# Kernel tuning notes

Hardware: AMD Instinct MI355X
Metric: run time of the kernel (lower is better)

## Reference

```python
import jax, jax.numpy as jnp
import numpy as np

N_NODES = 50000
N_EDGES = 800000
D = 128
N_GRAPHS = 64
N_CLASSES = 10


def setup_inputs() -> dict:
    key = jax.random.key(0)
    ks = jax.random.split(key, 10)
    x = jax.random.normal(ks[0], (N_NODES, D), dtype=jnp.float32)
    edge_index = jax.random.randint(ks[1], (2, N_EDGES), 0, N_NODES, dtype=jnp.int64)
    batch = jnp.sort(jax.random.randint(ks[2], (N_NODES,), 0, N_GRAPHS, dtype=jnp.int64))
    s = 1.0 / np.sqrt(D)
    W1a = jax.random.uniform(ks[3], (D, D), jnp.float32, -s, s)
    W1b = jax.random.uniform(ks[4], (D, D), jnp.float32, -s, s)
    W2a = jax.random.uniform(ks[5], (D, D), jnp.float32, -s, s)
    W2b = jax.random.uniform(ks[6], (D, D), jnp.float32, -s, s)
    Wfc = jax.random.uniform(ks[7], (D, N_CLASSES), jnp.float32, -s, s)
    return {
        "x": x, "edge_index": edge_index, "batch": batch,
        "W1a": W1a, "b1a": jnp.zeros((D,), jnp.float32),
        "W1b": W1b, "b1b": jnp.zeros((D,), jnp.float32),
        "W2a": W2a, "b2a": jnp.zeros((D,), jnp.float32),
        "W2b": W2b, "b2b": jnp.zeros((D,), jnp.float32),
        "Wfc": Wfc, "bfc": jnp.zeros((N_CLASSES,), jnp.float32),
    }


def _gin_conv(x, src, dst, Wa, ba, Wb, bb):
    # sum aggregation of neighbor messages x[src] into dst (eps = 0)
    agg = jax.ops.segment_sum(x[src], dst, num_segments=N_NODES)
    h = x + agg  # (1 + eps) * x + sum_{j->i} x_j
    h = jax.nn.relu(h @ Wa + ba)
    h = jax.nn.relu(h @ Wb + bb)
    return h


def reference(x, edge_index, batch, W1a, b1a, W1b, b1b, W2a, b2a, W2b, b2b, Wfc, bfc):
    src, dst = edge_index[0], edge_index[1]
    h = _gin_conv(x, src, dst, W1a, b1a, W1b, b1b)
    h = _gin_conv(h, src, dst, W2a, b2a, W2b, b2b)
    # global mean pool over graphs
    sums = jax.ops.segment_sum(h, batch, num_segments=N_GRAPHS)
    counts = jax.ops.segment_sum(jnp.ones((h.shape[0], 1), h.dtype), batch, num_segments=N_GRAPHS)
    pooled = sums / jnp.maximum(counts, 1.0)
    logits = pooled @ Wfc + bfc
    return jax.nn.sigmoid(logits)
```

## Files before the change

### kernel.cpp

```cpp
#include <hip/hip_runtime.h>

#define NN 50000
#define NE 800000
#define DF 128
#define NG 64
#define NC 10
#define NBK 98
#define PART_CHUNK 4096
#define PART_GRID 196
#define ACAP 12288
#define FINE_CAP 12288
#define RT 136
#define CAST_GRID 6250

typedef short bf16x8 __attribute__((ext_vector_type(8)));
typedef float f32x4  __attribute__((ext_vector_type(4)));

__device__ __forceinline__ void atomAddF(float* p, float v) {
  __hip_atomic_fetch_add(p, v, __ATOMIC_RELAXED, __HIP_MEMORY_SCOPE_AGENT);
}
__device__ __forceinline__ float b2f(unsigned short u) {
  union { unsigned int i; float f; } v; v.i = (unsigned int)u << 16; return v.f;
}
__device__ __forceinline__ unsigned int f2b(float f) {
  unsigned int i = __float_as_uint(f);
  return (i + 0x7fffu + ((i >> 16) & 1u)) >> 16;
}

__global__ __launch_bounds__(256) void k_prep(const float* __restrict__ x,
                                              unsigned short* __restrict__ xb,
                                              const float* __restrict__ W0,
                                              const float* __restrict__ W1,
                                              const float* __restrict__ W2,
                                              const float* __restrict__ W3,
                                              unsigned short* __restrict__ Wt)
{
  const int b = blockIdx.x;
  if (b < CAST_GRID) {
    const int i = b * 256 + threadIdx.x;
    const float4 v = reinterpret_cast<const float4*>(x)[i];
    uint2 o;
    o.x = f2b(v.x) | (f2b(v.y) << 16);
    o.y = f2b(v.z) | (f2b(v.w) << 16);
    reinterpret_cast<uint2*>(xb)[i] = o;
  } else {
    const int o = (b - CAST_GRID) * 256 + threadIdx.x;
    const int mat = o >> 11;
    const float* W = (mat == 0) ? W0 : (mat == 1) ? W1 : (mat == 2) ? W2 : W3;
    const int rem = o & 2047;
    const int kb = rem >> 7;
    const int n  = rem & 127;
    unsigned int u[8];
#pragma unroll
    for (int j = 0; j < 8; ++j) u[j] = f2b(W[(size_t)(kb * 8 + j) * DF + n]);
    uint4 p;
    p.x = u[0] | (u[1] << 16);
    p.y = u[2] | (u[3] << 16);
    p.z = u[4] | (u[5] << 16);
    p.w = u[6] | (u[7] << 16);
    *reinterpret_cast<uint4*>(Wt + (size_t)mat * DF * DF + (size_t)rem * 8) = p;
  }
}

__global__ __launch_bounds__(256) void k_part(const int* __restrict__ src,
                                              const int* __restrict__ dst,
                                              int* __restrict__ cnt_b,
                                              unsigned int* __restrict__ arena)
{
  __shared__ unsigned int stage[PART_CHUNK];
  __shared__ int lhist[128], lcnt[128], lcur[128], gbase[128];
  const int tid = threadIdx.x;
  const int e0  = blockIdx.x * PART_CHUNK;
  const int nE  = min(PART_CHUNK, NE - e0);

  for (int i = tid; i < 128; i += 256) lhist[i] = 0;
  __syncthreads();

  unsigned int pk[16];
  int bk[16];
#pragma unroll
  for (int i = 0; i < 16; ++i) {
    const int e = e0 + i * 256 + tid;
    if (e < NE) {
      const int d = dst[e];
      const int s = src[e];
      const int b = d >> 9;
      bk[i] = b;
      pk[i] = ((unsigned int)b << 25) | ((unsigned int)(d & 511) << 16) | (unsigned int)s;
      atomicAdd(&lhist[b], 1);
    } else {
      bk[i] = -1;
    }
  }
  __syncthreads();
  for (int i = tid; i < 128; i += 256) lcnt[i] = lhist[i];
  __syncthreads();
  for (int off = 1; off < 128; off <<= 1) {
    int v = 0;
    if (tid < 128 && tid >= off) v = lhist[tid - off];
    __syncthreads();
    if (tid < 128) lhist[tid] += v;
    __syncthreads();
  }
  if (tid < 128) lcur[tid] = lhist[tid] - lcnt[tid];
  __syncthreads();
#pragma unroll
  for (int i = 0; i < 16; ++i) {
    if (bk[i] >= 0) {
      const int pos = atomicAdd(&lcur[bk[i]], 1);
      stage[pos] = pk[i];
    }
  }
  __syncthreads();
  if (tid < NBK) {
    const int c = lcnt[tid];
    if (c > 0) gbase[tid] = atomicAdd(&cnt_b[tid], c);
  }
  __syncthreads();
  for (int idx = tid; idx < nE; idx += 256) {
    const unsigned int p = stage[idx];
    const int b = (int)(p >> 25);
    const int loff = lhist[b] - lcnt[b];
    arena[(size_t)b * ACAP + gbase[b] + (idx - loff)] = p;
  }
}

__global__ __launch_bounds__(128) void k_bscan(const int* __restrict__ cnt_b,
                                               int* __restrict__ base_b,
                                               int* __restrict__ rs)
{
  __shared__ int sm[128];
  const int t = threadIdx.x;
  const int v = (t < NBK) ? cnt_b[t] : 0;
  sm[t] = v;
  __syncthreads();
  for (int off = 1; off < 128; off <<= 1) {
    int u = (t >= off) ? sm[t - off] : 0;
    __syncthreads();
    sm[t] += u;
    __syncthreads();
  }
  base_b[t] = sm[t] - v;
  if (t == NBK - 1) rs[NN] = sm[t];
}

__global__ __launch_bounds__(256) void k_fine(const unsigned int* __restrict__ arena,
                                              const int* __restrict__ cnt_b,
                                              const int* __restrict__ base_b,
                                              int* __restrict__ rs,
                                              unsigned short* __restrict__ es)
{
  __shared__ unsigned short les[FINE_CAP];
  __shared__ int bins[4096];
  __shared__ int partials[256];
  const int tid   = threadIdx.x;
  const int b     = blockIdx.x;
  const int cnt   = cnt_b[b];
  const int wbase = base_b[b];
  const int nbase = b << 9;
  const int nwin  = min(512, NN - nbase);
  const unsigned int* ap = arena + (size_t)b * ACAP;

  for (int i = tid; i < 4096; i += 256) bins[i] = 0;
  __syncthreads();
  for (int idx = tid; idx < cnt; idx += 256) {
    const unsigned int p = ap[idx];
    const int key = (int)(((p >> 16) & 511) << 3) | (int)((p & 0xffffu) >> 13);
    atomicAdd(&bins[key], 1);
  }
  __syncthreads();
  const int b16 = tid * 16;
  int sum = 0;
#pragma unroll
  for (int k = 0; k < 16; ++k) sum += bins[b16 + k];
  partials[tid] = sum;
  __syncthreads();
  for (int off = 1; off < 256; off <<= 1) {
    int u = (tid >= off) ? partials[tid - off] : 0;
    __syncthreads();
    partials[tid] += u;
    __syncthreads();
  }
  int run = partials[tid] - sum;
#pragma unroll
  for (int k = 0; k < 16; ++k) {
    const int v = bins[b16 + k];
    bins[b16 + k] = run;
    run += v;
  }
  __syncthreads();
  for (int i = tid; i < nwin; i += 256) rs[nbase + i] = wbase + bins[i << 3];
  __syncthreads();
  if (cnt <= FINE_CAP) {
    for (int idx = tid; idx < cnt; idx += 256) {
      const unsigned int p = ap[idx];
      const int key = (int)(((p >> 16) & 511) << 3) | (int)((p & 0xffffu) >> 13);
      const int pos = atomicAdd(&bins[key], 1);
      les[pos] = (unsigned short)(p & 0xffffu);
    }
    __syncthreads();
    for (int i = tid; i < cnt; i += 256) es[wbase + i] = les[i];
  } else {
    for (int idx = tid; idx < cnt; idx += 256) {
      const unsigned int p = ap[idx];
      const int key = (int)(((p >> 16) & 511) << 3) | (int)((p & 0xffffu) >> 13);
      const int pos = atomicAdd(&bins[key], 1);
      es[wbase + pos] = (unsigned short)(p & 0xffffu);
    }
  }
}

__global__ __launch_bounds__(256) void k_gather(const unsigned short* __restrict__ feat,
                                                unsigned short* __restrict__ outp,
                                                const int* __restrict__ rs,
                                                const unsigned short* __restrict__ es)
{
  const int wid  = (blockIdx.x * 256 + threadIdx.x) >> 6;
  const int lane = threadIdx.x & 63;
  if (wid >= NN) return;
  const int beg = rs[wid];
  const int end = rs[wid + 1];
  const int off = lane * 2;

  const unsigned int self = *reinterpret_cast<const unsigned int*>(feat + (size_t)wid * DF + off);
  float ax = b2f(self & 0xffff), ay = b2f(self >> 16);
  int j = beg;
  while (j < end && (j & 3)) {
    const int s = es[j];
    const unsigned int u = *reinterpret_cast<const unsigned int*>(feat + (size_t)s * DF + off);
    ax += b2f(u & 0xffff);
    ay += b2f(u >> 16);
    ++j;
  }
  for (; j + 3 < end; j += 4) {
    const uint2 e4 = *reinterpret_cast<const uint2*>(es + j);
    const int s0 = (int)(e4.x & 0xffffu), s1 = (int)(e4.x >> 16);
    const int s2 = (int)(e4.y & 0xffffu), s3 = (int)(e4.y >> 16);
    const unsigned int u0 = *reinterpret_cast<const unsigned int*>(feat + (size_t)s0 * DF + off);
    const unsigned int u1 = *reinterpret_cast<const unsigned int*>(feat + (size_t)s1 * DF + off);
    const unsigned int u2 = *reinterpret_cast<const unsigned int*>(feat + (size_t)s2 * DF + off);
    const unsigned int u3 = *reinterpret_cast<const unsigned int*>(feat + (size_t)s3 * DF + off);
    ax += b2f(u0 & 0xffff) + b2f(u1 & 0xffff) + b2f(u2 & 0xffff) + b2f(u3 & 0xffff);
    ay += b2f(u0 >> 16)    + b2f(u1 >> 16)    + b2f(u2 >> 16)    + b2f(u3 >> 16);
  }
  for (; j < end; ++j) {
    const int s = es[j];
    const unsigned int u = *reinterpret_cast<const unsigned int*>(feat + (size_t)s * DF + off);
    ax += b2f(u & 0xffff);
    ay += b2f(u >> 16);
  }
  const unsigned int o = f2b(ax) | (f2b(ay) << 16);
  *reinterpret_cast<unsigned int*>(outp + (size_t)wid * DF + off) = o;
}

__global__ __launch_bounds__(256, 3) void k_gemm2(const unsigned short* __restrict__ Ab,
                                                  const unsigned short* __restrict__ Wta,
                                                  const float* __restrict__ ba,
                                                  const unsigned short* __restrict__ Wtb,
                                                  const float* __restrict__ bb,
                                                  unsigned short* __restrict__ outb, int M)
{
  __shared__ unsigned short WaL[2048 * 8];
  __shared__ unsigned short hL[4][16 * RT];
  const int tid  = threadIdx.x;
  const int lane = tid & 63;
  const int w    = tid >> 6;
  const int col  = lane & 15;
  const int kq   = lane >> 4;

#pragma unroll
  for (int i = 0; i < 8; ++i)
    *reinterpret_cast<uint4*>(&WaL[(i * 256 + tid) * 8]) =
        *reinterpret_cast<const uint4*>(&Wta[(size_t)(i * 256 + tid) * 8]);

  float4 bva[8], bvb[8];
#pragma unroll
  for (int nf = 0; nf < 8; ++nf) {
    bva[nf] = *reinterpret_cast<const float4*>(ba + nf * 16 + kq * 4);
    bvb[nf] = *reinterpret_cast<const float4*>(bb + nf * 16 + kq * 4);
  }

  const int m   = blockIdx.x * 64 + w * 16 + col;
  const int mld = (m < M) ? m : (M - 1);

  bf16x8 bc[4];
#pragma unroll
  for (int s = 0; s < 4; ++s)
    bc[s] = *reinterpret_cast<const bf16x8*>(Ab + (size_t)mld * DF + s * 32 + kq * 8);

  __syncthreads();

  f32x4 acc[8];
#pragma unroll
  for (int nf = 0; nf < 8; ++nf) acc[nf] = (f32x4){0.f, 0.f, 0.f, 0.f};
#pragma unroll
  for (int s = 0; s < 4; ++s) {
#pragma unroll
    for (int nf = 0; nf < 8; ++nf) {
      const bf16x8 wa = *reinterpret_cast<const bf16x8*>(
          &WaL[((s * 4 + kq) * 128 + nf * 16 + col) * 8]);
      acc[nf] = __builtin_amdgcn_mfma_f32_16x16x32_bf16(wa, bc[s], acc[nf], 0, 0, 0);
    }
  }

  unsigned short* hw = &hL[w][0];
#pragma unroll
  for (int nf = 0; nf < 8; ++nf) {
    uint2 pk;
    pk.x = f2b(fmaxf(acc[nf][0] + bva[nf].x, 0.f)) | (f2b(fmaxf(acc[nf][1] + bva[nf].y, 0.f)) << 16);
    pk.y = f2b(fmaxf(acc[nf][2] + bva[nf].z, 0.f)) | (f2b(fmaxf(acc[nf][3] + bva[nf].w, 0.f)) << 16);
    *reinterpret_cast<uint2*>(&hw[col * RT + nf * 16 + kq * 4]) = pk;
  }
  asm volatile("s_waitcnt lgkmcnt(0)" ::: "memory");
  __builtin_amdgcn_sched_barrier(0);

  f32x4 acc2[8];
#pragma unroll
  for (int nf = 0; nf < 8; ++nf) acc2[nf] = (f32x4){0.f, 0.f, 0.f, 0.f};
#pragma unroll
  for (int s = 0; s < 4; ++s) {
    const bf16x8 hb = *reinterpret_cast<const bf16x8*>(&hw[col * RT + s * 32 + kq * 8]);
#pragma unroll
    for (int nf = 0; nf < 8; ++nf) {
      const bf16x8 wb = *reinterpret_cast<const bf16x8*>(
          Wtb + ((size_t)(s * 4 + kq) * 128 + nf * 16 + col) * 8);
      acc2[nf] = __builtin_amdgcn_mfma_f32_16x16x32_bf16(wb, hb, acc2[nf], 0, 0, 0);
    }
  }
  if (m < M) {
#pragma unroll
    for (int nf = 0; nf < 8; ++nf) {
      ushort4 p;
      p.x = (unsigned short)f2b(fmaxf(acc2[nf][0] + bvb[nf].x, 0.f));
      p.y = (unsigned short)f2b(fmaxf(acc2[nf][1] + bvb[nf].y, 0.f));
      p.z = (unsigned short)f2b(fmaxf(acc2[nf][2] + bvb[nf].z, 0.f));
      p.w = (unsigned short)f2b(fmaxf(acc2[nf][3] + bvb[nf].w, 0.f));
      *reinterpret_cast<ushort4*>(outb + (size_t)m * DF + nf * 16 + kq * 4) = p;
    }
  }
}

__global__ __launch_bounds__(256) void k_pool(const unsigned short* __restrict__ h,
                                              const int* __restrict__ batch,
                                              float* __restrict__ sums,
                                              int* __restrict__ cnts)
{
  const int wv   = (blockIdx.x * 256 + threadIdx.x) >> 6;
  const int lane = threadIdx.x & 63;
  const int n0 = wv * 32;
  if (n0 >= NN) return;
  const int n1 = min(n0 + 32, NN);
  const int off = lane * 2;

  const int gfirst = batch[n0];
  const int glast  = batch[n1 - 1];
  float ax = 0.f, ay = 0.f;

  if (gfirst == glast) {
#pragma unroll 4
    for (int i = n0; i < n1; ++i) {
      const unsigned int u = *reinterpret_cast<const unsigned int*>(h + (size_t)i * DF + off);
      ax += b2f(u & 0xffff);
      ay += b2f(u >> 16);
    }
    atomAddF(&sums[gfirst * DF + off],     ax);
    atomAddF(&sums[gfirst * DF + off + 1], ay);
    if (lane == 0) atomicAdd(&cnts[gfirst], n1 - n0);
  } else {
    int g = gfirst, cnt = 0;
    for (int i = n0; i < n1; ++i) {
      const int gi = batch[i];
      if (gi != g) {
        atomAddF(&sums[g * DF + off],     ax);
        atomAddF(&sums[g * DF + off + 1], ay);
        if (lane == 0) atomicAdd(&cnts[g], cnt);
        ax = 0.f; ay = 0.f; cnt = 0; g = gi;
      }
      const unsigned int u = *reinterpret_cast<const unsigned int*>(h + (size_t)i * DF + off);
      ax += b2f(u & 0xffff);
      ay += b2f(u >> 16);
      ++cnt;
    }
    atomAddF(&sums[g * DF + off],     ax);
    atomAddF(&sums[g * DF + off + 1], ay);
    if (lane == 0) atomicAdd(&cnts[g], cnt);
  }
}

__global__ __launch_bounds__(256) void k_head(const float* __restrict__ sums,
                                              const int* __restrict__ cnts,
                                              const float* __restrict__ Wfc,
                                              const float* __restrict__ bfc,
                                              float* __restrict__ out)
{
  for (int o = threadIdx.x; o < NG * NC; o += 256) {
    const int g = o / NC, c = o % NC;
    const float inv = 1.f / fmaxf((float)cnts[g], 1.f);
    float z = bfc[c];
    for (int k = 0; k < DF; ++k)
      z = fmaf(sums[g * DF + k] * inv, Wfc[k * NC + c], z);
    out[o] = 1.f / (1.f + expf(-z));
  }
}

extern "C" void kernel_launch(void* const* d_in, const int* in_sizes, int n_in,
                              void* d_out, int out_size, void* d_ws, size_t ws_size,
                              hipStream_t stream)
{
  const float* x   = (const float*)d_in[0];
  const int*   ei  = (const int*)d_in[1];
  const int* batch = (const int*)d_in[2];
  const float* W1a = (const float*)d_in[3];
  const float* b1a = (const float*)d_in[4];
  const float* W1b = (const float*)d_in[5];
  const float* b1b = (const float*)d_in[6];
  const float* W2a = (const float*)d_in[7];
  const float* b2a = (const float*)d_in[8];
  const float* W2b = (const float*)d_in[9];
  const float* b2b = (const float*)d_in[10];
  const float* Wfc = (const float*)d_in[11];
  const float* bfc = (const float*)d_in[12];
  float* out = (float*)d_out;

  const int* src = ei;
  const int* dst = ei + NE;

  unsigned short* xb = (unsigned short*)d_ws;
  unsigned short* A  = xb + (size_t)NN * DF;
  unsigned short* H  = A + (size_t)NN * DF;
  unsigned short* Wt = H + (size_t)NN * DF;
  float* sums  = (float*)(Wt + (size_t)4 * DF * DF);
  int*   cnts  = (int*)(sums + NG * DF);
  int*   cnt_b = cnts + 64;
  int*   base_b= cnt_b + 128;
  int*   rs    = base_b + 128;
  unsigned short* es = (unsigned short*)(rs + (NN + 4));
  unsigned int* arena = (unsigned int*)(es + NE);

  unsigned short* Wt1a = Wt;
  unsigned short* Wt1b = Wt + DF * DF;
  unsigned short* Wt2a = Wt + 2 * DF * DF;
  unsigned short* Wt2b = Wt + 3 * DF * DF;

  const int gemm_grid   = (NN + 63) / 64;
  const int gather_grid = (NN * 64 + 255) / 256;
  const int pool_grid   = ((NN + 31) / 32 + 3) / 4;

  k_prep<<<CAST_GRID + 32, 256, 0, stream>>>(x, xb, W1a, W1b, W2a, W2b, Wt);
  hipMemsetAsync(sums, 0, (size_t)(NG * DF + 64 + 128) * sizeof(float), stream);
  k_part<<<PART_GRID, 256, 0, stream>>>(src, dst, cnt_b, arena);
  k_bscan<<<1, 128, 0, stream>>>(cnt_b, base_b, rs);
  k_fine<<<NBK, 256, 0, stream>>>(arena, cnt_b, base_b, rs, es);

  k_gather<<<gather_grid, 256, 0, stream>>>(xb, A, rs, es);
  k_gemm2<<<gemm_grid, 256, 0, stream>>>(A, Wt1a, b1a, Wt1b, b1b, A, NN);

  k_gather<<<gather_grid, 256, 0, stream>>>(A, H, rs, es);
  k_gemm2<<<gemm_grid, 256, 0, stream>>>(H, Wt2a, b2a, Wt2b, b2b, H, NN);

  k_pool<<<pool_grid, 256, 0, stream>>>(H, batch, sums, cnts);
  k_head<<<1, 256, 0, stream>>>(sums, cnts, Wfc, bfc, out);
}
```

Before: 192.9 us.

## Fuse all pipeline stages into one cooperative persistent kernel with grid syncs

Replaces the sequence of separate kernel launches (prep, partition, bucket scan, fine sort, two gather+GEMM layers, pool, head) with a single cooperative persistent kernel that loops over virtual blocks and separates phases with grid-wide syncs. The bucket prefix scan is folded into each fine-sort block, and the GEMM phase loads the weight tile once per persistent block and loops over row tiles. The aim is to remove launch gaps and per-block weight reloads. In exchange, grid size is capped by occupancy of the combined kernel, whose shared-memory footprint is the largest phase union. This may reduce parallelism and latency hiding in the gather phases, and grid syncs add their own cost. A fallback multi-kernel path is kept in case the cooperative launch fails.

```diff
diff --git a/kernel.cpp b/kernel.cpp
--- a/kernel.cpp
+++ b/kernel.cpp
@@ -1,4 +1,6 @@
 #include <hip/hip_runtime.h>
+#include <hip/hip_cooperative_groups.h>
+namespace cg = cooperative_groups;
 
 #define NN 50000
 #define NE 800000
@@ -12,6 +14,7 @@
 #define FINE_CAP 12288
 #define RT 136
 #define CAST_GRID 6250
+#define GEMM_TILES 782
 
 typedef short bf16x8 __attribute__((ext_vector_type(8)));
 typedef float f32x4  __attribute__((ext_vector_type(4)));
@@ -27,29 +30,37 @@
   return (i + 0x7fffu + ((i >> 16) & 1u)) >> 16;
 }
 
-__global__ __launch_bounds__(256) void k_prep(const float* __restrict__ x,
-                                              unsigned short* __restrict__ xb,
-                                              const float* __restrict__ W0,
-                                              const float* __restrict__ W1,
-                                              const float* __restrict__ W2,
-                                              const float* __restrict__ W3,
-                                              unsigned short* __restrict__ Wt)
-{
-  const int b = blockIdx.x;
-  if (b < CAST_GRID) {
-    const int i = b * 256 + threadIdx.x;
-    const float4 v = reinterpret_cast<const float4*>(x)[i];
+struct KArgs {
+  const float* x; const int* src; const int* dst; const int* batch;
+  const float *W1a, *b1a, *W1b, *b1b, *W2a, *b2a, *W2b, *b2b, *Wfc, *bfc;
+  float* out;
+  unsigned short *xb, *A, *H, *Wt;
+  float* sums; int* cnts; int* cnt_b; int* rs;
+  unsigned short* es; unsigned int* arena;
+};
+
+struct SmU {
+  union {
+    struct { unsigned int stage[PART_CHUNK]; int lhist[128]; int lcnt[128]; int lcur[128]; int gbase[128]; } part;
+    struct { unsigned short les[FINE_CAP]; int bins[4096]; int partials[256]; int basebuf[128]; } fine;
+    struct { unsigned short WaL[2048 * 8]; unsigned short hL[4][16 * RT]; } gemm;
+  };
+};
+
+__device__ __forceinline__ void d_prep(int vb, const KArgs& a, int tid) {
+  if (vb < CAST_GRID) {
+    const int i = vb * 256 + tid;
+    const float4 v = reinterpret_cast<const float4*>(a.x)[i];
     uint2 o;
     o.x = f2b(v.x) | (f2b(v.y) << 16);
     o.y = f2b(v.z) | (f2b(v.w) << 16);
-    reinterpret_cast<uint2*>(xb)[i] = o;
+    reinterpret_cast<uint2*>(a.xb)[i] = o;
   } else {
-    const int o = (b - CAST_GRID) * 256 + threadIdx.x;
+    const int o = (vb - CAST_GRID) * 256 + tid;
     const int mat = o >> 11;
-    const float* W = (mat == 0) ? W0 : (mat == 1) ? W1 : (mat == 2) ? W2 : W3;
+    const float* W = (mat == 0) ? a.W1a : (mat == 1) ? a.W1b : (mat == 2) ? a.W2a : a.W2b;
     const int rem = o & 2047;
-    const int kb = rem >> 7;
-    const int n  = rem & 127;
+    const int kb = rem >> 7, n = rem & 127;
     unsigned int u[8];
 #pragma unroll
     for (int j = 0; j < 8; ++j) u[j] = f2b(W[(size_t)(kb * 8 + j) * DF + n]);
@@ -58,178 +69,136 @@
     p.y = u[2] | (u[3] << 16);
     p.z = u[4] | (u[5] << 16);
     p.w = u[6] | (u[7] << 16);
-    *reinterpret_cast<uint4*>(Wt + (size_t)mat * DF * DF + (size_t)rem * 8) = p;
-  }
-}
-
-__global__ __launch_bounds__(256) void k_part(const int* __restrict__ src,
-                                              const int* __restrict__ dst,
-                                              int* __restrict__ cnt_b,
-                                              unsigned int* __restrict__ arena)
-{
-  __shared__ unsigned int stage[PART_CHUNK];
-  __shared__ int lhist[128], lcnt[128], lcur[128], gbase[128];
-  const int tid = threadIdx.x;
-  const int e0  = blockIdx.x * PART_CHUNK;
-  const int nE  = min(PART_CHUNK, NE - e0);
-
-  for (int i = tid; i < 128; i += 256) lhist[i] = 0;
-  __syncthreads();
-
-  unsigned int pk[16];
-  int bk[16];
+    *reinterpret_cast<uint4*>(a.Wt + (size_t)mat * DF * DF + (size_t)rem * 8) = p;
+  }
+}
+
+__device__ void d_part(int vb, const KArgs& a, SmU& sm, int tid) {
+  const int e0 = vb * PART_CHUNK;
+  const int nE = min(PART_CHUNK, NE - e0);
+  for (int i = tid; i < 128; i += 256) sm.part.lhist[i] = 0;
+  __syncthreads();
+  unsigned int pk[16]; int bk[16];
 #pragma unroll
   for (int i = 0; i < 16; ++i) {
     const int e = e0 + i * 256 + tid;
     if (e < NE) {
-      const int d = dst[e];
-      const int s = src[e];
+      const int d = a.dst[e], s = a.src[e];
       const int b = d >> 9;
       bk[i] = b;
       pk[i] = ((unsigned int)b << 25) | ((unsigned int)(d & 511) << 16) | (unsigned int)s;
-      atomicAdd(&lhist[b], 1);
-    } else {
-      bk[i] = -1;
-    }
-  }
-  __syncthreads();
-  for (int i = tid; i < 128; i += 256) lcnt[i] = lhist[i];
+      atomicAdd(&sm.part.lhist[b], 1);
+    } else bk[i] = -1;
+  }
+  __syncthreads();
+  for (int i = tid; i < 128; i += 256) sm.part.lcnt[i] = sm.part.lhist[i];
   __syncthreads();
   for (int off = 1; off < 128; off <<= 1) {
     int v = 0;
-    if (tid < 128 && tid >= off) v = lhist[tid - off];
-    __syncthreads();
-    if (tid < 128) lhist[tid] += v;
-    __syncthreads();
-  }
-  if (tid < 128) lcur[tid] = lhist[tid] - lcnt[tid];
-  __syncthreads();
-#pragma unroll
-  for (int i = 0; i < 16; ++i) {
+    if (tid < 128 && tid >= off) v = sm.part.lhist[tid - off];
+    __syncthreads();
+    if (tid < 128) sm.part.lhist[tid] += v;
+    __syncthreads();
+  }
+  if (tid < 128) sm.part.lcur[tid] = sm.part.lhist[tid] - sm.part.lcnt[tid];
+  __syncthreads();
+#pragma unroll
+  for (int i = 0; i < 16; ++i)
     if (bk[i] >= 0) {
-      const int pos = atomicAdd(&lcur[bk[i]], 1);
-      stage[pos] = pk[i];
-    }
-  }
+      const int pos = atomicAdd(&sm.part.lcur[bk[i]], 1);
+      sm.part.stage[pos] = pk[i];
+    }
   __syncthreads();
   if (tid < NBK) {
-    const int c = lcnt[tid];
-    if (c > 0) gbase[tid] = atomicAdd(&cnt_b[tid], c);
+    const int c = sm.part.lcnt[tid];
+    if (c > 0) sm.part.gbase[tid] = atomicAdd(&a.cnt_b[tid], c);
   }
   __syncthreads();
   for (int idx = tid; idx < nE; idx += 256) {
-    const unsigned int p = stage[idx];
+    const unsigned int p = sm.part.stage[idx];
     const int b = (int)(p >> 25);
-    const int loff = lhist[b] - lcnt[b];
-    arena[(size_t)b * ACAP + gbase[b] + (idx - loff)] = p;
-  }
-}
-
-__global__ __launch_bounds__(128) void k_bscan(const int* __restrict__ cnt_b,
-                                               int* __restrict__ base_b,
-                                               int* __restrict__ rs)
-{
-  __shared__ int sm[128];
-  const int t = threadIdx.x;
-  const int v = (t < NBK) ? cnt_b[t] : 0;
-  sm[t] = v;
+    const int loff = sm.part.lhist[b] - sm.part.lcnt[b];
+    a.arena[(size_t)b * ACAP + sm.part.gbase[b] + (idx - loff)] = p;
+  }
+}
+
+__device__ void d_fine(int b, const KArgs& a, SmU& sm, int tid) {
+  int v0 = 0;
+  if (tid < 128) { v0 = (tid < NBK) ? a.cnt_b[tid] : 0; sm.fine.basebuf[tid] = v0; }
   __syncthreads();
   for (int off = 1; off < 128; off <<= 1) {
-    int u = (t >= off) ? sm[t - off] : 0;
-    __syncthreads();
-    sm[t] += u;
-    __syncthreads();
-  }
-  base_b[t] = sm[t] - v;
-  if (t == NBK - 1) rs[NN] = sm[t];
-}
-
-__global__ __launch_bounds__(256) void k_fine(const unsigned int* __restrict__ arena,
-                                              const int* __restrict__ cnt_b,
-                                              const int* __restrict__ base_b,
-                                              int* __restrict__ rs,
-                                              unsigned short* __restrict__ es)
-{
-  __shared__ unsigned short les[FINE_CAP];
-  __shared__ int bins[4096];
-  __shared__ int partials[256];
-  const int tid   = threadIdx.x;
-  const int b     = blockIdx.x;
-  const int cnt   = cnt_b[b];
-  const int wbase = base_b[b];
+    int u = 0;
+    if (tid < 128 && tid >= off) u = sm.fine.basebuf[tid - off];
+    __syncthreads();
+    if (tid < 128) sm.fine.basebuf[tid] += u;
+    __syncthreads();
+  }
+  const int wbase = (b == 0) ? 0 : sm.fine.basebuf[b - 1];
+  const int cnt = a.cnt_b[b];
   const int nbase = b << 9;
-  const int nwin  = min(512, NN - nbase);
-  const unsigned int* ap = arena + (size_t)b * ACAP;
-
-  for (int i = tid; i < 4096; i += 256) bins[i] = 0;
+  const int nwin = min(512, NN - nbase);
+  const unsigned int* ap = a.arena + (size_t)b * ACAP;
+
+  for (int i = tid; i < 4096; i += 256) sm.fine.bins[i] = 0;
   __syncthreads();
   for (int idx = tid; idx < cnt; idx += 256) {
     const unsigned int p = ap[idx];
     const int key = (int)(((p >> 16) & 511) << 3) | (int)((p & 0xffffu) >> 13);
-    atomicAdd(&bins[key], 1);
+    atomicAdd(&sm.fine.bins[key], 1);
   }
   __syncthreads();
   const int b16 = tid * 16;
   int sum = 0;
 #pragma unroll
-  for (int k = 0; k < 16; ++k) sum += bins[b16 + k];
-  partials[tid] = sum;
+  for (int k = 0; k < 16; ++k) sum += sm.fine.bins[b16 + k];
+  sm.fine.partials[tid] = sum;
   __syncthreads();
   for (int off = 1; off < 256; off <<= 1) {
-    int u = (tid >= off) ? partials[tid - off] : 0;
-    __syncthreads();
-    partials[tid] += u;
-    __syncthreads();
-  }
-  int run = partials[tid] - sum;
+    int u = (tid >= off) ? sm.fine.partials[tid - off] : 0;
+    __syncthreads();
+    sm.fine.partials[tid] += u;
+    __syncthreads();
+  }
+  int run = sm.fine.partials[tid] - sum;
 #pragma unroll
   for (int k = 0; k < 16; ++k) {
-    const int v = bins[b16 + k];
-    bins[b16 + k] = run;
+    const int v = sm.fine.bins[b16 + k];
+    sm.fine.bins[b16 + k] = run;
     run += v;
   }
   __syncthreads();
-  for (int i = tid; i < nwin; i += 256) rs[nbase + i] = wbase + bins[i << 3];
+  for (int i = tid; i < nwin; i += 256) a.rs[nbase + i] = wbase + sm.fine.bins[i << 3];
   __syncthreads();
   if (cnt <= FINE_CAP) {
     for (int idx = tid; idx < cnt; idx += 256) {
       const unsigned int p = ap[idx];
       const int key = (int)(((p >> 16) & 511) << 3) | (int)((p & 0xffffu) >> 13);
-      const int pos = atomicAdd(&bins[key], 1);
-      les[pos] = (unsigned short)(p & 0xffffu);
-    }
-    __syncthreads();
-    for (int i = tid; i < cnt; i += 256) es[wbase + i] = les[i];
+      const int pos = atomicAdd(&sm.fine.bins[key], 1);
+      sm.fine.les[pos] = (unsigned short)(p & 0xffffu);
+    }
+    __syncthreads();
+    for (int i = tid; i < cnt; i += 256) a.es[wbase + i] = sm.fine.les[i];
   } else {
     for (int idx = tid; idx < cnt; idx += 256) {
       const unsigned int p = ap[idx];
       const int key = (int)(((p >> 16) & 511) << 3) | (int)((p & 0xffffu) >> 13);
-      const int pos = atomicAdd(&bins[key], 1);
-      es[wbase + pos] = (unsigned short)(p & 0xffffu);
-    }
-  }
-}
-
-__global__ __launch_bounds__(256) void k_gather(const unsigned short* __restrict__ feat,
-                                                unsigned short* __restrict__ outp,
-                                                const int* __restrict__ rs,
-                                                const unsigned short* __restrict__ es)
-{
-  const int wid  = (blockIdx.x * 256 + threadIdx.x) >> 6;
-  const int lane = threadIdx.x & 63;
-  if (wid >= NN) return;
+      const int pos = atomicAdd(&sm.fine.bins[key], 1);
+      a.es[wbase + pos] = (unsigned short)(p & 0xffffu);
+    }
+  }
+}
+
+__device__ void d_gather(int wid, const unsigned short* feat, unsigned short* outp,
+                         const int* rs, const unsigned short* es, int lane) {
   const int beg = rs[wid];
   const int end = rs[wid + 1];
   const int off = lane * 2;
-
   const unsigned int self = *reinterpret_cast<const unsigned int*>(feat + (size_t)wid * DF + off);
   float ax = b2f(self & 0xffff), ay = b2f(self >> 16);
   int j = beg;
   while (j < end && (j & 3)) {
-    const int s = es[j];
-    const unsigned int u = *reinterpret_cast<const unsigned int*>(feat + (size_t)s * DF + off);
-    ax += b2f(u & 0xffff);
-    ay += b2f(u >> 16);
+    const unsigned int u = *reinterpret_cast<const unsigned int*>(feat + (size_t)es[j] * DF + off);
+    ax += b2f(u & 0xffff); ay += b2f(u >> 16);
     ++j;
   }
   for (; j + 3 < end; j += 4) {
@@ -244,34 +213,24 @@
     ay += b2f(u0 >> 16)    + b2f(u1 >> 16)    + b2f(u2 >> 16)    + b2f(u3 >> 16);
   }
   for (; j < end; ++j) {
-    const int s = es[j];
-    const unsigned int u = *reinterpret_cast<const unsigned int*>(feat + (size_t)s * DF + off);
-    ax += b2f(u & 0xffff);
-    ay += b2f(u >> 16);
+    const unsigned int u = *reinterpret_cast<const unsigned int*>(feat + (size_t)es[j] * DF + off);
+    ax += b2f(u & 0xffff); ay += b2f(u >> 16);
   }
   const unsigned int o = f2b(ax) | (f2b(ay) << 16);
   *reinterpret_cast<unsigned int*>(outp + (size_t)wid * DF + off) = o;
 }
 
-__global__ __launch_bounds__(256, 3) void k_gemm2(const unsigned short* __restrict__ Ab,
-                                                  const unsigned short* __restrict__ Wta,
-                                                  const float* __restrict__ ba,
-                                                  const unsigned short* __restrict__ Wtb,
-                                                  const float* __restrict__ bb,
-                                                  unsigned short* __restrict__ outb, int M)
-{
-  __shared__ unsigned short WaL[2048 * 8];
-  __shared__ unsigned short hL[4][16 * RT];
-  const int tid  = threadIdx.x;
+__device__ void d_gemm_phase(const unsigned short* Ab, const unsigned short* Wta,
+                             const float* ba, const unsigned short* Wtb, const float* bb,
+                             unsigned short* outb, SmU& sm, int bid, int nb, int tid) {
   const int lane = tid & 63;
-  const int w    = tid >> 6;
-  const int col  = lane & 15;
-  const int kq   = lane >> 4;
-
-#pragma unroll
-  for (int i = 0; i < 8; ++i)
-    *reinterpret_cast<uint4*>(&WaL[(i * 256 + tid) * 8]) =
-        *reinterpret_cast<const uint4*>(&Wta[(size_t)(i * 256 + tid) * 8]);
+  const int w = tid >> 6;
+  const int col = lane & 15;
+  const int kq = lane >> 4;
+
+  for (int i = tid; i < 2048; i += 256)
+    *reinterpret_cast<uint4*>(&sm.gemm.WaL[i * 8]) =
+        *reinterpret_cast<const uint4*>(&Wta[(size_t)i * 8]);
 
   float4 bva[8], bvb[8];
 #pragma unroll
@@ -279,128 +238,170 @@
     bva[nf] = *reinterpret_cast<const float4*>(ba + nf * 16 + kq * 4);
     bvb[nf] = *reinterpret_cast<const float4*>(bb + nf * 16 + kq * 4);
   }
-
-  const int m   = blockIdx.x * 64 + w * 16 + col;
-  const int mld = (m < M) ? m : (M - 1);
-
-  bf16x8 bc[4];
-#pragma unroll
-  for (int s = 0; s < 4; ++s)
-    bc[s] = *reinterpret_cast<const bf16x8*>(Ab + (size_t)mld * DF + s * 32 + kq * 8);
-
-  __syncthreads();
-
-  f32x4 acc[8];
-#pragma unroll
-  for (int nf = 0; nf < 8; ++nf) acc[nf] = (f32x4){0.f, 0.f, 0.f, 0.f};
-#pragma unroll
-  for (int s = 0; s < 4; ++s) {
+  __syncthreads();
+
+  unsigned short* hw = &sm.gemm.hL[w][0];
+  for (int t = bid; t < GEMM_TILES; t += nb) {
+    const int m = t * 64 + w * 16 + col;
+    const int mld = (m < NN) ? m : (NN - 1);
+    bf16x8 bc[4];
+#pragma unroll
+    for (int s = 0; s < 4; ++s)
+      bc[s] = *reinterpret_cast<const bf16x8*>(Ab + (size_t)mld * DF + s * 32 + kq * 8);
+
+    f32x4 acc[8];
+#pragma unroll
+    for (int nf = 0; nf < 8; ++nf) acc[nf] = (f32x4){0.f, 0.f, 0.f, 0.f};
+#pragma unroll
+    for (int s = 0; s < 4; ++s) {
+#pragma unroll
+      for (int nf = 0; nf < 8; ++nf) {
+        const bf16x8 wa = *reinterpret_cast<const bf16x8*>(
+            &sm.gemm.WaL[((s * 4 + kq) * 128 + nf * 16 + col) * 8]);
+        acc[nf] = __builtin_amdgcn_mfma_f32_16x16x32_bf16(wa, bc[s], acc[nf], 0, 0, 0);
+      }
+    }
 #pragma unroll
     for (int nf = 0; nf < 8; ++nf) {
-      const bf16x8 wa = *reinterpret_cast<const bf16x8*>(
-          &WaL[((s * 4 + kq) * 128 + nf * 16 + col) * 8]);
-      acc[nf] = __builtin_amdgcn_mfma_f32_16x16x32_bf16(wa, bc[s], acc[nf], 0, 0, 0);
-    }
-  }
-
-  unsigned short* hw = &hL[w][0];
-#pragma unroll
-  for (int nf = 0; nf < 8; ++nf) {
-    uint2 pk;
-    pk.x = f2b(fmaxf(acc[nf][0] + bva[nf].x, 0.f)) | (f2b(fmaxf(acc[nf][1] + bva[nf].y, 0.f)) << 16);
-    pk.y = f2b(fmaxf(acc[nf][2] + bva[nf].z, 0.f)) | (f2b(fmaxf(acc[nf][3] + bva[nf].w, 0.f)) << 16);
-    *reinterpret_cast<uint2*>(&hw[col * RT + nf * 16 + kq * 4]) = pk;
-  }
-  asm volatile("s_waitcnt lgkmcnt(0)" ::: "memory");
-  __builtin_amdgcn_sched_barrier(0);
-
-  f32x4 acc2[8];
-#pragma unroll
-  for (int nf = 0; nf < 8; ++nf) acc2[nf] = (f32x4){0.f, 0.f, 0.f, 0.f};
-#pragma unroll
-  for (int s = 0; s < 4; ++s) {
-    const bf16x8 hb = *reinterpret_cast<const bf16x8*>(&hw[col * RT + s * 32 + kq * 8]);
-#pragma unroll
-    for (int nf = 0; nf < 8; ++nf) {
-      const bf16x8 wb = *reinterpret_cast<const bf16x8*>(
-          Wtb + ((size_t)(s * 4 + kq) * 128 + nf * 16 + col) * 8);
-      acc2[nf] = __builtin_amdgcn_mfma_f32_16x16x32_bf16(wb, hb, acc2[nf], 0, 0, 0);
-    }
-  }
-  if (m < M) {
-#pragma unroll
-    for (int nf = 0; nf < 8; ++nf) {
-      ushort4 p;
-      p.x = (unsigned short)f2b(fmaxf(acc2[nf][0] + bvb[nf].x, 0.f));
-      p.y = (unsigned short)f2b(fmaxf(acc2[nf][1] + bvb[nf].y, 0.f));
-      p.z = (unsigned short)f2b(fmaxf(acc2[nf][2] + bvb[nf].z, 0.f));
-      p.w = (unsigned short)f2b(fmaxf(acc2[nf][3] + bvb[nf].w, 0.f));
-      *reinterpret_cast<ushort4*>(outb + (size_t)m * DF + nf * 16 + kq * 4) = p;
-    }
-  }
-}
-
-__global__ __launch_bounds__(256) void k_pool(const unsigned short* __restrict__ h,
-                                              const int* __restrict__ batch,
-                                              float* __restrict__ sums,
-                                              int* __restrict__ cnts)
-{
-  const int wv   = (blockIdx.x * 256 + threadIdx.x) >> 6;
-  const int lane = threadIdx.x & 63;
+      uint2 pk;
+      pk.x = f2b(fmaxf(acc[nf][0] + bva[nf].x, 0.f)) | (f2b(fmaxf(acc[nf][1] + bva[nf].y, 0.f)) << 16);
+      pk.y = f2b(fmaxf(acc[nf][2] + bva[nf].z, 0.f)) | (f2b(fmaxf(acc[nf][3] + bva[nf].w, 0.f)) << 16);
+      *reinterpret_cast<uint2*>(&hw[col * RT + nf * 16 + kq * 4]) = pk;
+    }
+    asm volatile("s_waitcnt lgkmcnt(0)" ::: "memory");
+    __builtin_amdgcn_sched_barrier(0);
+
+    f32x4 acc2[8];
+#pragma unroll
+    for (int nf = 0; nf < 8; ++nf) acc2[nf] = (f32x4){0.f, 0.f, 0.f, 0.f};
+#pragma unroll
+    for (int s = 0; s < 4; ++s) {
+      const bf16x8 hb = *reinterpret_cast<const bf16x8*>(&hw[col * RT + s * 32 + kq * 8]);
+#pragma unroll
+      for (int nf = 0; nf < 8; ++nf) {
+        const bf16x8 wb = *reinterpret_cast<const bf16x8*>(
+            Wtb + ((size_t)(s * 4 + kq) * 128 + nf * 16 + col) * 8);
+        acc2[nf] = __builtin_amdgcn_mfma_f32_16x16x32_bf16(wb, hb, acc2[nf], 0, 0, 0);
+      }
+    }
+    if (m < NN) {
+#pragma unroll
+      for (int nf = 0; nf < 8; ++nf) {
+        ushort4 p;
+        p.x = (unsigned short)f2b(fmaxf(acc2[nf][0] + bvb[nf].x, 0.f));
+        p.y = (unsigned short)f2b(fmaxf(acc2[nf][1] + bvb[nf].y, 0.f));
+        p.z = (unsigned short)f2b(fmaxf(acc2[nf][2] + bvb[nf].z, 0.f));
+        p.w = (unsigned short)f2b(fmaxf(acc2[nf][3] + bvb[nf].w, 0.f));
+        *reinterpret_cast<ushort4*>(outb + (size_t)m * DF + nf * 16 + kq * 4) = p;
+      }
+    }
+  }
+}
+
+__device__ void d_pool(int wv, const KArgs& a, int lane) {
   const int n0 = wv * 32;
-  if (n0 >= NN) return;
   const int n1 = min(n0 + 32, NN);
   const int off = lane * 2;
-
-  const int gfirst = batch[n0];
-  const int glast  = batch[n1 - 1];
+  const int gfirst = a.batch[n0];
+  const int glast = a.batch[n1 - 1];
   float ax = 0.f, ay = 0.f;
-
   if (gfirst == glast) {
 #pragma unroll 4
     for (int i = n0; i < n1; ++i) {
-      const unsigned int u = *reinterpret_cast<const unsigned int*>(h + (size_t)i * DF + off);
-      ax += b2f(u & 0xffff);
-      ay += b2f(u >> 16);
-    }
-    atomAddF(&sums[gfirst * DF + off],     ax);
-    atomAddF(&sums[gfirst * DF + off + 1], ay);
-    if (lane == 0) atomicAdd(&cnts[gfirst], n1 - n0);
+      const unsigned int u = *reinterpret_cast<const unsigned int*>(a.H + (size_t)i * DF + off);
+      ax += b2f(u & 0xffff); ay += b2f(u >> 16);
+    }
+    atomAddF(&a.sums[gfirst * DF + off], ax);
+    atomAddF(&a.sums[gfirst * DF + off + 1], ay);
+    if (lane == 0) atomicAdd(&a.cnts[gfirst], n1 - n0);
   } else {
     int g = gfirst, cnt = 0;
     for (int i = n0; i < n1; ++i) {
-      const int gi = batch[i];
+      const int gi = a.batch[i];
       if (gi != g) {
-        atomAddF(&sums[g * DF + off],     ax);
-        atomAddF(&sums[g * DF + off + 1], ay);
-        if (lane == 0) atomicAdd(&cnts[g], cnt);
+        atomAddF(&a.sums[g * DF + off], ax);
+        atomAddF(&a.sums[g * DF + off + 1], ay);
+        if (lane == 0) atomicAdd(&a.cnts[g], cnt);
         ax = 0.f; ay = 0.f; cnt = 0; g = gi;
       }
-      const unsigned int u = *reinterpret_cast<const unsigned int*>(h + (size_t)i * DF + off);
-      ax += b2f(u & 0xffff);
-      ay += b2f(u >> 16);
+      const unsigned int u = *reinterpret_cast<const unsigned int*>(a.H + (size_t)i * DF + off);
+      ax += b2f(u & 0xffff); ay += b2f(u >> 16);
       ++cnt;
     }
-    atomAddF(&sums[g * DF + off],     ax);
-    atomAddF(&sums[g * DF + off + 1], ay);
-    if (lane == 0) atomicAdd(&cnts[g], cnt);
-  }
-}
-
-__global__ __launch_bounds__(256) void k_head(const float* __restrict__ sums,
-                                              const int* __restrict__ cnts,
-                                              const float* __restrict__ Wfc,
-                                              const float* __restrict__ bfc,
-                                              float* __restrict__ out)
-{
-  for (int o = threadIdx.x; o < NG * NC; o += 256) {
+    atomAddF(&a.sums[g * DF + off], ax);
+    atomAddF(&a.sums[g * DF + off + 1], ay);
+    if (lane == 0) atomicAdd(&a.cnts[g], cnt);
+  }
+}
+
+__device__ void d_head(const KArgs& a, int tid) {
+  for (int o = tid; o < NG * NC; o += 256) {
     const int g = o / NC, c = o % NC;
-    const float inv = 1.f / fmaxf((float)cnts[g], 1.f);
-    float z = bfc[c];
+    const float inv = 1.f / fmaxf((float)a.cnts[g], 1.f);
+    float z = a.bfc[c];
     for (int k = 0; k < DF; ++k)
-      z = fmaf(sums[g * DF + k] * inv, Wfc[k * NC + c], z);
-    out[o] = 1.f / (1.f + expf(-z));
-  }
+      z = fmaf(a.sums[g * DF + k] * inv, a.Wfc[k * NC + c], z);
+    a.out[o] = 1.f / (1.f + expf(-z));
+  }
+}
+
+__global__ __launch_bounds__(256) void k_mega(KArgs a) {
+  __shared__ SmU sm;
+  const int tid = threadIdx.x;
+  const int bid = blockIdx.x;
+  const int nb = gridDim.x;
+  cg::grid_group gg = cg::this_grid();
+  const int gw = (bid * 256 + tid) >> 6;
+  const int nw = nb * 4;
+
+  for (int vb = bid; vb < CAST_GRID + 32; vb += nb) d_prep(vb, a, tid);
+  for (int vb = bid; vb < PART_GRID; vb += nb) { d_part(vb, a, sm, tid); __syncthreads(); }
+  gg.sync();
+  if (bid == 0 && tid == 0) a.rs[NN] = NE;
+  for (int b = bid; b < NBK; b += nb) { d_fine(b, a, sm, tid); __syncthreads(); }
+  gg.sync();
+  for (int wid = gw; wid < NN; wid += nw) d_gather(wid, a.xb, a.A, a.rs, a.es, tid & 63);
+  gg.sync();
+  d_gemm_phase(a.A, a.Wt, a.b1a, a.Wt + DF * DF, a.b1b, a.A, sm, bid, nb, tid);
+  gg.sync();
+  for (int wid = gw; wid < NN; wid += nw) d_gather(wid, a.A, a.H, a.rs, a.es, tid & 63);
+  gg.sync();
+  d_gemm_phase(a.H, a.Wt + 2 * DF * DF, a.b2a, a.Wt + 3 * DF * DF, a.b2b, a.H, sm, bid, nb, tid);
+  gg.sync();
+  for (int wv = gw; wv < (NN + 31) / 32; wv += nw) d_pool(wv, a, tid & 63);
+  gg.sync();
+  if (bid == 0) d_head(a, tid);
+}
+
+__global__ __launch_bounds__(256) void w_prep(KArgs a) {
+  for (int vb = blockIdx.x; vb < CAST_GRID + 32; vb += gridDim.x) d_prep(vb, a, threadIdx.x);
+}
+__global__ __launch_bounds__(256) void w_part(KArgs a) {
+  __shared__ SmU sm;
+  for (int vb = blockIdx.x; vb < PART_GRID; vb += gridDim.x) { d_part(vb, a, sm, threadIdx.x); __syncthreads(); }
+}
+__global__ __launch_bounds__(256) void w_fine(KArgs a) {
+  __shared__ SmU sm;
+  if (blockIdx.x == 0 && threadIdx.x == 0) a.rs[NN] = NE;
+  for (int b = blockIdx.x; b < NBK; b += gridDim.x) { d_fine(b, a, sm, threadIdx.x); __syncthreads(); }
+}
+__global__ __launch_bounds__(256) void w_gather(const unsigned short* feat, unsigned short* outp,
+                                                const int* rs, const unsigned short* es) {
+  const int wid = (blockIdx.x * 256 + threadIdx.x) >> 6;
+  if (wid < NN) d_gather(wid, feat, outp, rs, es, threadIdx.x & 63);
+}
+__global__ __launch_bounds__(256) void w_gemm(const unsigned short* Ab, const unsigned short* Wta,
+                                              const float* ba, const unsigned short* Wtb,
+                                              const float* bb, unsigned short* outb) {
+  __shared__ SmU sm;
+  d_gemm_phase(Ab, Wta, ba, Wtb, bb, outb, sm, blockIdx.x, gridDim.x, threadIdx.x);
+}
+__global__ __launch_bounds__(256) void w_pool(KArgs a) {
+  const int wv = (blockIdx.x * 256 + threadIdx.x) >> 6;
+  if (wv < (NN + 31) / 32) d_pool(wv, a, threadIdx.x & 63);
+}
+__global__ __launch_bounds__(256) void w_head(KArgs a) {
+  if (blockIdx.x == 0) d_head(a, threadIdx.x);
 }
 
 extern "C" void kernel_launch(void* const* d_in, const int* in_sizes, int n_in,
@@ -410,20 +411,6 @@
   const float* x   = (const float*)d_in[0];
   const int*   ei  = (const int*)d_in[1];
   const int* batch = (const int*)d_in[2];
-  const float* W1a = (const float*)d_in[3];
-  const float* b1a = (const float*)d_in[4];
-  const float* W1b = (const float*)d_in[5];
-  const float* b1b = (const float*)d_in[6];
-  const float* W2a = (const float*)d_in[7];
-  const float* b2a = (const float*)d_in[8];
-  const float* W2b = (const float*)d_in[9];
-  const float* b2b = (const float*)d_in[10];
-  const float* Wfc = (const float*)d_in[11];
-  const float* bfc = (const float*)d_in[12];
-  float* out = (float*)d_out;
-
-  const int* src = ei;
-  const int* dst = ei + NE;
 
   unsigned short* xb = (unsigned short*)d_ws;
   unsigned short* A  = xb + (size_t)NN * DF;
@@ -432,32 +419,41 @@
   float* sums  = (float*)(Wt + (size_t)4 * DF * DF);
   int*   cnts  = (int*)(sums + NG * DF);
   int*   cnt_b = cnts + 64;
-  int*   base_b= cnt_b + 128;
-  int*   rs    = base_b + 128;
+  int*   rs    = cnt_b + 128;
   unsigned short* es = (unsigned short*)(rs + (NN + 4));
   unsigned int* arena = (unsigned int*)(es + NE);
 
-  unsigned short* Wt1a = Wt;
-  unsigned short* Wt1b = Wt + DF * DF;
-  unsigned short* Wt2a = Wt + 2 * DF * DF;
-  unsigned short* Wt2b = Wt + 3 * DF * DF;
-
-  const int gemm_grid   = (NN + 63) / 64;
-  const int gather_grid = (NN * 64 + 255) / 256;
-  const int pool_grid   = ((NN + 31) / 32 + 3) / 4;
-
-  k_prep<<<CAST_GRID + 32, 256, 0, stream>>>(x, xb, W1a, W1b, W2a, W2b, Wt);
+  KArgs ka;
+  ka.x = x; ka.src = ei; ka.dst = ei + NE; ka.batch = batch;
+  ka.W1a = (const float*)d_in[3];  ka.b1a = (const float*)d_in[4];
+  ka.W1b = (const float*)d_in[5];  ka.b1b = (const float*)d_in[6];
+  ka.W2a = (const float*)d_in[7];  ka.b2a = (const float*)d_in[8];
+  ka.W2b = (const float*)d_in[9];  ka.b2b = (const float*)d_in[10];
+  ka.Wfc = (const float*)d_in[11]; ka.bfc = (const float*)d_in[12];
+  ka.out = (float*)d_out;
+  ka.xb = xb; ka.A = A; ka.H = H; ka.Wt = Wt;
+  ka.sums = sums; ka.cnts = cnts; ka.cnt_b = cnt_b; ka.rs = rs;
+  ka.es = es; ka.arena = arena;
+
   hipMemsetAsync(sums, 0, (size_t)(NG * DF + 64 + 128) * sizeof(float), stream);
-  k_part<<<PART_GRID, 256, 0, stream>>>(src, dst, cnt_b, arena);
-  k_bscan<<<1, 128, 0, stream>>>(cnt_b, base_b, rs);
-  k_fine<<<NBK, 256, 0, stream>>>(arena, cnt_b, base_b, rs, es);
-
-  k_gather<<<gather_grid, 256, 0, stream>>>(xb, A, rs, es);
-  k_gemm2<<<gemm_grid, 256, 0, stream>>>(A, Wt1a, b1a, Wt1b, b1b, A, NN);
-
-  k_gather<<<gather_grid, 256, 0, stream>>>(A, H, rs, es);
-  k_gemm2<<<gemm_grid, 256, 0, stream>>>(H, Wt2a, b2a, Wt2b, b2b, H, NN);
-
-  k_pool<<<pool_grid, 256, 0, stream>>>(H, batch, sums, cnts);
-  k_head<<<1, 256, 0, stream>>>(sums, cnts, Wfc, bfc, out);
-}
+
+  int occ = 0;
+  hipError_t oe = hipOccupancyMaxActiveBlocksPerMultiprocessor(&occ, k_mega, 256, 0);
+  if (oe != hipSuccess || occ < 1) occ = 1;
+  const int grid = occ * 256;
+
+  void* params[] = { (void*)&ka };
+  hipError_t rc = hipLaunchCooperativeKernel((void*)k_mega, dim3(grid), dim3(256),
+                                             params, 0, stream);
+  if (rc != hipSuccess) {
+    w_prep<<<CAST_GRID + 32, 256, 0, stream>>>(ka);
+    w_part<<<PART_GRID, 256, 0, stream>>>(ka);
+    w_fine<<<NBK, 256, 0, stream>>>(ka);
+    w_gather<<<(NN * 64 + 255) / 256, 256, 0, stream>>>(xb, A, rs, es);
+    w_gemm<<<GEMM_TILES, 256, 0, stream>>>(A, Wt, ka.b1a, Wt + DF * DF, ka.b1b, A);
+    w_gather<<<(NN * 64 + 255) / 256, 256, 0, stream>>>(A, H, rs, es);
+    w_gemm<<<GEMM_TILES, 256, 0, stream>>>(H, Wt + 2 * DF * DF, ka.b2a, Wt + 3 * DF * DF, ka.b2b, H);
+    w_pool<<<((NN + 31) / 32 + 3) / 4, 256, 0, stream>>>(ka);
+    w_head<<<1, 256, 0, stream>>>(ka);
+  }
+}
```

Result: slower. 674.4 us (+249.6%).
